# Kernel tuning notes

Measured on AMD Instinct MI355X. Metric: run time of the kernel, lower is better.

The kernel has to match this reference:

```python
import jax, jax.numpy as jnp
import numpy as np

NQ = 12          # qubits per node circuit
DIM = 2 ** NQ    # statevector length 4096


def _apply_1q(state, U, w):
    """Apply 2x2 gate U (shared (2,2) or per-batch (B,2,2)) on wire w. state: (B, 4096)."""
    B = state.shape[0]
    l, r = 2 ** w, 2 ** (NQ - w - 1)
    s = state.reshape(B, l, 2, r)
    if U.ndim == 2:
        s = jnp.einsum('ij,bajc->baic', U, s)
    else:
        s = jnp.einsum('bij,bajc->baic', U, s)
    return s.reshape(B, DIM)


_G = np.zeros((2, 2, 2, 2), np.complex64)  # CNOT tensor: (c_out, t_out, c_in, t_in)
for _c in range(2):
    for _t in range(2):
        _G[_c, _t ^ _c, _c, _t] = 1.0


def _apply_cnot(state, c, t):
    B = state.shape[0]
    lo, hi = min(c, t), max(c, t)
    a, m, r = 2 ** lo, 2 ** (hi - lo - 1), 2 ** (NQ - hi - 1)
    s = state.reshape(B, a, 2, m, 2, r)
    T = _G if c == lo else _G.transpose(1, 0, 3, 2)  # reorder to (lo, hi) axis convention
    s = jnp.einsum('ijkl,bakcld->baicjd', jnp.asarray(T), s)
    return s.reshape(B, DIM)


def _ry_mats(ang):
    """Per-node RY matrices. ang: (B,) -> (B,2,2) complex64."""
    c, s = jnp.cos(ang / 2), jnp.sin(ang / 2)
    U = jnp.stack([jnp.stack([c, -s], -1), jnp.stack([s, c], -1)], -2)
    return U.astype(jnp.complex64)


def _rot_mat(p):
    """PennyLane Rot(phi, theta, omega) = RZ(omega) RY(theta) RZ(phi)."""
    phi, th, om = p[0], p[1], p[2]
    c, s = jnp.cos(th / 2), jnp.sin(th / 2)
    U = jnp.stack([
        jnp.stack([jnp.exp(-0.5j * (phi + om)) * c, -jnp.exp(0.5j * (phi - om)) * s]),
        jnp.stack([jnp.exp(-0.5j * (phi - om)) * s, jnp.exp(0.5j * (phi + om)) * c]),
    ])
    return U.astype(jnp.complex64)


# (rot_wire_a, rot_wire_b, (cnot_control, cnot_target)) blocks of the TTN circuit
_BLOCKS = [(0, 1, (0, 1)), (2, 3, (3, 2)), (4, 5, (4, 5)), (6, 7, (7, 6)),
           (8, 9, (8, 9)), (10, 11, (11, 10)), (1, 2, (1, 2)), (5, 6, (6, 5)),
           (9, 10, (10, 9)), (2, 5, (2, 5)), (5, 9, (5, 9))]


def _ttn_circuit(M, theta):
    """Batched 12-qubit TTN circuit. M: (B,12) angles, theta: (69,). Returns <Z_9>: (B,)."""
    B = M.shape[0]
    state = jnp.zeros((B, DIM), jnp.complex64).at[:, 0].set(1.0)
    for w in range(NQ):
        state = _apply_1q(state, _ry_mats(M[:, w]), w)
    k = 0
    for w1, w2, (c, t) in _BLOCKS:
        state = _apply_1q(state, _rot_mat(theta[3 * k:3 * k + 3]), w1); k += 1
        state = _apply_1q(state, _rot_mat(theta[3 * k:3 * k + 3]), w2); k += 1
        state = _apply_cnot(state, c, t)
    state = _apply_1q(state, _rot_mat(theta[3 * k:3 * k + 3]), 4)  # final Rot, k = 22
    probs = (state.real ** 2 + state.imag ** 2).reshape(B, 2 ** 9, 2, 2 ** 2)
    return probs[:, :, 0].sum((1, 2)) - probs[:, :, 1].sum((1, 2))  # <Z on wire 9>


def setup_inputs() -> dict:
    key = jax.random.key(0)
    kx, ke, ki, ko, kt = jax.random.split(key, 5)
    N, E, D = 1024, 8192, 4
    X = jax.random.normal(kx, (N, D), dtype=jnp.float32)
    e = jax.random.uniform(ke, (E,), dtype=jnp.float32)
    idx_i = jax.random.randint(ki, (E,), 0, N)
    idx_o = jax.random.randint(ko, (E,), 0, N)
    Ri = jnp.zeros((N, E), jnp.float32).at[idx_i, jnp.arange(E)].set(1.0)
    Ro = jnp.zeros((N, E), jnp.float32).at[idx_o, jnp.arange(E)].set(1.0)
    theta = jax.random.uniform(kt, (69,), dtype=jnp.float32, maxval=2 * np.pi)
    return {"X": X, "e": e, "Ri": Ri, "Ro": Ro, "theta": theta}


def reference(X, e, Ri, Ro, theta):
    bo = Ro.T @ X                     # [E, D] features of outgoing nodes
    bi = Ri.T @ X                     # [E, D]
    mi = (Ri * e) @ bo                # [N, D] edge-weighted aggregation
    mo = (Ro * e) @ bi                # [N, D]
    M = jnp.concatenate([mi, mo, X], axis=1)   # [N, 12] -> circuit angles
    z = _ttn_circuit(M, theta)
    return (jnp.pi * (1.0 - z)).astype(jnp.float32)  # 2*pi*(1 - <Z>)/2 per node
```

## Files before the change

### kernel.cpp

```cpp
#include <hip/hip_runtime.h>
#include <math.h>

#define NN 1024
#define NE 8192

struct c32 { float x, y; };
__device__ __forceinline__ c32 cmul(c32 a, c32 b)  { return {a.x*b.x - a.y*b.y, a.x*b.y + a.y*b.x}; }
__device__ __forceinline__ c32 cmulc(c32 a, c32 b) { return {a.x*b.x + a.y*b.y, a.y*b.x - a.x*b.y}; }
__device__ __forceinline__ c32 cadd(c32 a, c32 b)  { return {a.x + b.x, a.y + b.y}; }

__device__ __forceinline__ float sx(float v, int m)  { return __shfl_xor(v, m, 64); }
__device__ __forceinline__ float sidx(float v, int l){ return __shfl(v, l, 64); }

__device__ __forceinline__ void rot2(const float* __restrict__ t3, c32 A[2][2]) {
  float phi = t3[0], th = t3[1], om = t3[2];
  float s, c;   sincosf(0.5f * th, &s, &c);
  float sa, ca; sincosf(0.5f * (phi + om), &sa, &ca);
  float sb, cb; sincosf(0.5f * (phi - om), &sb, &cb);
  A[0][0] = {  ca * c, -sa * c };
  A[0][1] = { -cb * s, -sb * s };
  A[1][0] = {  cb * s, -sb * s };
  A[1][1] = {  ca * c,  sa * c };
}

__global__ void k_extract(const float* __restrict__ Ri, const float* __restrict__ Ro,
                          int* __restrict__ idx_i, int* __restrict__ idx_o,
                          float* __restrict__ mimo) {
  const int per = NN * NE / 4;
  int tid    = blockIdx.x * blockDim.x + threadIdx.x;
  int stride = gridDim.x * blockDim.x;
  if (tid < (2 * NN * 4) / 4) ((float4*)mimo)[tid] = make_float4(0.f, 0.f, 0.f, 0.f);
  for (int t = tid; t < 2 * per; t += stride) {
    bool first = (t < per);
    const float4* src = first ? (const float4*)Ri : (const float4*)Ro;
    int* dst          = first ? idx_i : idx_o;
    int q = first ? t : t - per;
    float4 v = src[q];
    if (v.x != 0.f || v.y != 0.f || v.z != 0.f || v.w != 0.f) {
      int base = q * 4;
      int n = base >> 13;
      int k = base & (NE - 1);
      if (v.x != 0.f) dst[k + 0] = n;
      if (v.y != 0.f) dst[k + 1] = n;
      if (v.z != 0.f) dst[k + 2] = n;
      if (v.w != 0.f) dst[k + 3] = n;
    }
  }
}

__global__ void k_edges(const float* __restrict__ X, const float* __restrict__ e,
                        const int* __restrict__ idx_i, const int* __restrict__ idx_o,
                        float* __restrict__ mi, float* __restrict__ mo) {
  int k = blockIdx.x * blockDim.x + threadIdx.x;
  if (k >= NE) return;
  int ni = idx_i[k], no = idx_o[k];
  float w = e[k];
  float4 xo = ((const float4*)X)[no];
  float4 xi = ((const float4*)X)[ni];
  atomicAdd(&mi[ni * 4 + 0], w * xo.x);
  atomicAdd(&mi[ni * 4 + 1], w * xo.y);
  atomicAdd(&mi[ni * 4 + 2], w * xo.z);
  atomicAdd(&mi[ni * 4 + 3], w * xo.w);
  atomicAdd(&mo[no * 4 + 0], w * xi.x);
  atomicAdd(&mo[no * 4 + 1], w * xi.y);
  atomicAdd(&mo[no * 4 + 2], w * xi.z);
  atomicAdd(&mo[no * 4 + 3], w * xi.w);
}

__device__ __forceinline__ void rot_lane(c32* a, const c32 (*U)[2], int lane, int b) {
  int s = (lane >> b) & 1;
  c32 us = s ? U[1][1] : U[0][0];
  c32 up = s ? U[1][0] : U[0][1];
  #pragma unroll
  for (int r = 0; r < 4; r++) {
    c32 p = { sx(a[r].x, 1 << b), sx(a[r].y, 1 << b) };
    a[r] = cadd(cmul(us, a[r]), cmul(up, p));
  }
}

__device__ __forceinline__ void rot_pair(c32& x0, c32& x1, const c32 (*U)[2]) {
  c32 n0 = cadd(cmul(U[0][0], x0), cmul(U[0][1], x1));
  c32 n1 = cadd(cmul(U[1][0], x0), cmul(U[1][1], x1));
  x0 = n0; x1 = n1;
}

__device__ __forceinline__ void cnot_ll(c32* a, int lane, int c, int t) {
  int idx = lane ^ (((lane >> c) & 1) << t);
  #pragma unroll
  for (int r = 0; r < 4; r++) a[r] = { sidx(a[r].x, idx), sidx(a[r].y, idx) };
}

__device__ __forceinline__ void rotB(c32* bb, const c32 (*U)[2], int k) {
  int mask = (1 << k) - 1;
  #pragma unroll
  for (int t = 0; t < 8; t++) {
    int i0 = ((t & ~mask) << 1) | (t & mask);
    int i1 = i0 | (1 << k);
    c32 b0 = bb[i0], b1 = bb[i1];
    bb[i0] = cadd(cmul(U[0][0], b0), cmul(U[0][1], b1));
    bb[i1] = cadd(cmul(U[1][0], b0), cmul(U[1][1], b1));
  }
}

__device__ __forceinline__ void cnotB(c32* bb, int c, int t) {
  int lo = c < t ? c : t, hi = c < t ? t : c;
  int lm = (1 << lo) - 1, hm = (1 << hi) - 1;
  #pragma unroll
  for (int q = 0; q < 4; q++) {
    int x = ((q & ~lm) << 1) | (q & lm);
    x = ((x & ~hm) << 1) | (x & hm);
    int i0 = x | (1 << c), i1 = i0 | (1 << t);
    c32 tmp = bb[i0]; bb[i0] = bb[i1]; bb[i1] = tmp;
  }
}

__global__ void __launch_bounds__(64) k_sv3(const float* __restrict__ X,
                                            const float* __restrict__ theta,
                                            const float* __restrict__ mi,
                                            const float* __restrict__ mo,
                                            float* __restrict__ out) {
  __shared__ c32 R[23][2][2];
  const int lane = threadIdx.x;
  const int n = blockIdx.x;

  if (lane < 23) {
    c32 A[2][2];
    rot2(theta + 3 * lane, A);
    R[lane][0][0] = A[0][0]; R[lane][0][1] = A[0][1];
    R[lane][1][0] = A[1][0]; R[lane][1][1] = A[1][1];
  }

  float4 miv = ((const float4*)mi)[n];
  float4 mov = ((const float4*)mo)[n];
  float4 xv  = ((const float4*)X)[n];
  float ang[12] = { miv.x, miv.y, miv.z, miv.w, mov.x, mov.y, mov.z, mov.w, xv.x, xv.y, xv.z, xv.w };
  float cw[12], sw[12];
  #pragma unroll
  for (int w = 0; w < 12; w++) __sincosf(0.5f * ang[w], &sw[w], &cw[w]);

  c32 a[4];
  {
    float lfac = 1.f;
    #pragma unroll
    for (int w = 2; w < 8; w++) lfac *= ((lane >> (7 - w)) & 1) ? sw[w] : cw[w];
    a[0] = { cw[0] * cw[1] * lfac, 0.f };
    a[1] = { cw[0] * sw[1] * lfac, 0.f };
    a[2] = { sw[0] * cw[1] * lfac, 0.f };
    a[3] = { sw[0] * sw[1] * lfac, 0.f };
  }
  c32 bb[16];
  #pragma unroll
  for (int i = 0; i < 16; i++) {
    float amp = 1.f;
    #pragma unroll
    for (int w = 8; w < 12; w++) amp *= ((i >> (11 - w)) & 1) ? sw[w] : cw[w];
    bb[i] = { amp, 0.f };
  }
  __syncthreads();

  rot_pair(a[0], a[2], R[0]);  rot_pair(a[1], a[3], R[0]);
  rot_pair(a[0], a[1], R[1]);  rot_pair(a[2], a[3], R[1]);
  { c32 t = a[2]; a[2] = a[3]; a[3] = t; }
  rot_lane(a, R[2], lane, 5);
  rot_lane(a, R[3], lane, 4);
  cnot_ll(a, lane, 4, 5);
  rot_lane(a, R[4], lane, 3);
  rot_lane(a, R[5], lane, 2);
  cnot_ll(a, lane, 3, 2);
  rot_lane(a, R[6], lane, 1);
  rot_lane(a, R[7], lane, 0);
  cnot_ll(a, lane, 0, 1);
  rot_pair(a[0], a[1], R[12]); rot_pair(a[2], a[3], R[12]);
  rot_lane(a, R[13], lane, 5);
  a[1] = { sx(a[1].x, 32), sx(a[1].y, 32) };
  a[3] = { sx(a[3].x, 32), sx(a[3].y, 32) };
  rot_lane(a, R[14], lane, 2);
  rot_lane(a, R[15], lane, 1);
  cnot_ll(a, lane, 1, 2);
  rot_lane(a, R[18], lane, 5);
  rot_lane(a, R[19], lane, 2);
  cnot_ll(a, lane, 5, 2);
  rot_lane(a, R[22], lane, 3);

  rotB(bb, R[8], 3);  rotB(bb, R[9], 2);  cnotB(bb, 3, 2);
  rotB(bb, R[10], 1); rotB(bb, R[11], 0); cnotB(bb, 0, 1);
  rotB(bb, R[16], 2); rotB(bb, R[17], 1); cnotB(bb, 1, 2);

  int s5 = (lane >> 2) & 1;
  float p00 = 0.f, p11 = 0.f; c32 p01 = {0.f, 0.f};
  #pragma unroll
  for (int r = 0; r < 4; r++) {
    c32 pr = { sx(a[r].x, 4), sx(a[r].y, 4) };
    float nn = a[r].x * a[r].x + a[r].y * a[r].y;
    c32 cp = cmulc(a[r], pr);
    p00 += s5 ? 0.f : nn;
    p11 += s5 ? nn : 0.f;
    p01.x += s5 ? 0.f : cp.x;
    p01.y += s5 ? 0.f : cp.y;
  }
  #pragma unroll
  for (int m = 1; m < 64; m <<= 1) {
    p00 += sx(p00, m); p11 += sx(p11, m);
    p01.x += sx(p01.x, m); p01.y += sx(p01.y, m);
  }

  float q00 = 0.f, q11 = 0.f; c32 q01 = {0.f, 0.f};
  #pragma unroll
  for (int ao = 0; ao < 8; ao++) {
    int i0 = ((ao & ~3) << 1) | (ao & 3);
    int i1 = i0 | 4;
    c32 b0 = bb[i0], b1 = bb[i1];
    q00 += b0.x * b0.x + b0.y * b0.y;
    q11 += b1.x * b1.x + b1.y * b1.y;
    q01 = cadd(q01, cmulc(b0, b1));
  }

  c32 U4[4][4];
  #pragma unroll
  for (int i = 0; i < 2; i++)
    #pragma unroll
    for (int p = 0; p < 2; p++)
      #pragma unroll
      for (int j = 0; j < 2; j++)
        #pragma unroll
        for (int q = 0; q < 2; q++)
          U4[2 * i + p][2 * j + q] = cmul(R[20][i][j], R[21][p][q]);
  #pragma unroll
  for (int c = 0; c < 4; c++) { c32 t = U4[2][c]; U4[2][c] = U4[3][c]; U4[3][c] = t; }

  c32 rho5[2][2] = { {{p00, 0.f}, p01}, {{p01.x, -p01.y}, {p11, 0.f}} };
  c32 rho9[2][2] = { {{q00, 0.f}, q01}, {{q01.x, -q01.y}, {q11, 0.f}} };
  float z = 0.f;
  #pragma unroll
  for (int aa = 0; aa < 4; aa++)
    #pragma unroll
    for (int b2 = 0; b2 < 4; b2++) {
      c32 m = {0.f, 0.f};
      #pragma unroll
      for (int i = 0; i < 4; i++) {
        c32 t = cmulc(U4[i][aa], U4[i][b2]);
        if (i & 1) { m.x -= t.x; m.y -= t.y; } else { m = cadd(m, t); }
      }
      c32 rr = cmul(rho5[aa >> 1][b2 >> 1], rho9[aa & 1][b2 & 1]);
      z += m.x * rr.x - m.y * rr.y;
    }

  if (lane == 0) out[n] = 3.14159265358979f * (1.f - z);
}

extern "C" void kernel_launch(void* const* d_in, const int* in_sizes, int n_in,
                              void* d_out, int out_size, void* d_ws, size_t ws_size,
                              hipStream_t stream) {
  (void)in_sizes; (void)n_in; (void)out_size; (void)ws_size;
  const float* X     = (const float*)d_in[0];
  const float* e     = (const float*)d_in[1];
  const float* Ri    = (const float*)d_in[2];
  const float* Ro    = (const float*)d_in[3];
  const float* theta = (const float*)d_in[4];
  float* out = (float*)d_out;

  char* ws = (char*)d_ws;
  int*   idx_i = (int*)(ws);
  int*   idx_o = (int*)(ws + 32768);
  float* mi    = (float*)(ws + 65536);
  float* mo    = (float*)(ws + 65536 + 16384);

  hipLaunchKernelGGL(k_extract, dim3(4096), dim3(256), 0, stream, Ri, Ro, idx_i, idx_o, mi);
  hipLaunchKernelGGL(k_edges,   dim3(NE / 256), dim3(256), 0, stream, X, e, idx_i, idx_o, mi, mo);
  hipLaunchKernelGGL(k_sv3,     dim3(NN), dim3(64), 0, stream, X, theta, mi, mo, out);
}
```

Measured before the change: 40.16 us.

## Fuse extract, edge aggregation and statevector kernels into one cooperative kernel

Replaces the three launches with a single cooperative kernel of 256 blocks that use grid.sync between phases. While scanning Ri and Ro, the kernel pairs each edge's in- and out-node with an atomicExch slot, so the edge aggregation happens inline and the separate index arrays go away. It then runs the circuit with four nodes per 256-thread block. This removes launch gaps and an intermediate pass, but adds grid-wide syncs, atomic exchanges and atomic reads, and uses a smaller grid than before for the dense 64MB scan.

Result: slower. 143.2 us (+256.5%).

```diff
diff --git a/kernel.cpp b/kernel.cpp
--- a/kernel.cpp
+++ b/kernel.cpp
@@ -1,5 +1,8 @@
 #include <hip/hip_runtime.h>
+#include <hip/hip_cooperative_groups.h>
 #include <math.h>
+
+namespace cg = cooperative_groups;
 
 #define NN 1024
 #define NE 8192
@@ -23,50 +26,6 @@
   A[1][1] = {  ca * c,  sa * c };
 }
 
-__global__ void k_extract(const float* __restrict__ Ri, const float* __restrict__ Ro,
-                          int* __restrict__ idx_i, int* __restrict__ idx_o,
-                          float* __restrict__ mimo) {
-  const int per = NN * NE / 4;
-  int tid    = blockIdx.x * blockDim.x + threadIdx.x;
-  int stride = gridDim.x * blockDim.x;
-  if (tid < (2 * NN * 4) / 4) ((float4*)mimo)[tid] = make_float4(0.f, 0.f, 0.f, 0.f);
-  for (int t = tid; t < 2 * per; t += stride) {
-    bool first = (t < per);
-    const float4* src = first ? (const float4*)Ri : (const float4*)Ro;
-    int* dst          = first ? idx_i : idx_o;
-    int q = first ? t : t - per;
-    float4 v = src[q];
-    if (v.x != 0.f || v.y != 0.f || v.z != 0.f || v.w != 0.f) {
-      int base = q * 4;
-      int n = base >> 13;
-      int k = base & (NE - 1);
-      if (v.x != 0.f) dst[k + 0] = n;
-      if (v.y != 0.f) dst[k + 1] = n;
-      if (v.z != 0.f) dst[k + 2] = n;
-      if (v.w != 0.f) dst[k + 3] = n;
-    }
-  }
-}
-
-__global__ void k_edges(const float* __restrict__ X, const float* __restrict__ e,
-                        const int* __restrict__ idx_i, const int* __restrict__ idx_o,
-                        float* __restrict__ mi, float* __restrict__ mo) {
-  int k = blockIdx.x * blockDim.x + threadIdx.x;
-  if (k >= NE) return;
-  int ni = idx_i[k], no = idx_o[k];
-  float w = e[k];
-  float4 xo = ((const float4*)X)[no];
-  float4 xi = ((const float4*)X)[ni];
-  atomicAdd(&mi[ni * 4 + 0], w * xo.x);
-  atomicAdd(&mi[ni * 4 + 1], w * xo.y);
-  atomicAdd(&mi[ni * 4 + 2], w * xo.z);
-  atomicAdd(&mi[ni * 4 + 3], w * xo.w);
-  atomicAdd(&mo[no * 4 + 0], w * xi.x);
-  atomicAdd(&mo[no * 4 + 1], w * xi.y);
-  atomicAdd(&mo[no * 4 + 2], w * xi.z);
-  atomicAdd(&mo[no * 4 + 3], w * xi.w);
-}
-
 __device__ __forceinline__ void rot_lane(c32* a, const c32 (*U)[2], int lane, int b) {
   int s = (lane >> b) & 1;
   c32 us = s ? U[1][1] : U[0][0];
@@ -77,19 +36,16 @@
     a[r] = cadd(cmul(us, a[r]), cmul(up, p));
   }
 }
-
 __device__ __forceinline__ void rot_pair(c32& x0, c32& x1, const c32 (*U)[2]) {
   c32 n0 = cadd(cmul(U[0][0], x0), cmul(U[0][1], x1));
   c32 n1 = cadd(cmul(U[1][0], x0), cmul(U[1][1], x1));
   x0 = n0; x1 = n1;
 }
-
 __device__ __forceinline__ void cnot_ll(c32* a, int lane, int c, int t) {
   int idx = lane ^ (((lane >> c) & 1) << t);
   #pragma unroll
   for (int r = 0; r < 4; r++) a[r] = { sidx(a[r].x, idx), sidx(a[r].y, idx) };
 }
-
 __device__ __forceinline__ void rotB(c32* bb, const c32 (*U)[2], int k) {
   int mask = (1 << k) - 1;
   #pragma unroll
@@ -101,7 +57,6 @@
     bb[i1] = cadd(cmul(U[1][0], b0), cmul(U[1][1], b1));
   }
 }
-
 __device__ __forceinline__ void cnotB(c32* bb, int c, int t) {
   int lo = c < t ? c : t, hi = c < t ? t : c;
   int lm = (1 << lo) - 1, hm = (1 << hi) - 1;
@@ -114,29 +69,124 @@
   }
 }
 
-__global__ void __launch_bounds__(64) k_sv3(const float* __restrict__ X,
-                                            const float* __restrict__ theta,
-                                            const float* __restrict__ mi,
-                                            const float* __restrict__ mo,
-                                            float* __restrict__ out) {
+__device__ __forceinline__ void scanq(float4 v, int q, const float* __restrict__ e,
+                                      const float* __restrict__ X,
+                                      int* __restrict__ slot, float* __restrict__ mimo,
+                                      bool isRo) {
+  if (v.x == 0.f && v.y == 0.f && v.z == 0.f && v.w == 0.f) return;
+  int n = q >> 11;
+  int k = (q << 2) & (NE - 1);
+  float vv[4] = { v.x, v.y, v.z, v.w };
+  #pragma unroll
+  for (int c = 0; c < 4; c++) if (vv[c] != 0.f) {
+    int kk = k + c;
+    int old = atomicExch(&slot[kk], n);
+    if (old >= 0) {
+      float w = e[kk];
+      int ni = isRo ? old : n;
+      int no = isRo ? n : old;
+      float4 xo = ((const float4*)X)[no];
+      float4 xi = ((const float4*)X)[ni];
+      atomicAdd(&mimo[ni * 4 + 0], w * xo.x);
+      atomicAdd(&mimo[ni * 4 + 1], w * xo.y);
+      atomicAdd(&mimo[ni * 4 + 2], w * xo.z);
+      atomicAdd(&mimo[ni * 4 + 3], w * xo.w);
+      atomicAdd(&mimo[4096 + no * 4 + 0], w * xi.x);
+      atomicAdd(&mimo[4096 + no * 4 + 1], w * xi.y);
+      atomicAdd(&mimo[4096 + no * 4 + 2], w * xi.z);
+      atomicAdd(&mimo[4096 + no * 4 + 3], w * xi.w);
+    }
+  }
+}
+
+__global__ void __launch_bounds__(256) k_all(const float* __restrict__ X,
+                                             const float* __restrict__ e,
+                                             const float* __restrict__ Ri,
+                                             const float* __restrict__ Ro,
+                                             const float* __restrict__ theta,
+                                             float* __restrict__ out,
+                                             int* __restrict__ slot,
+                                             float* __restrict__ mimo) {
+  cg::grid_group grid = cg::this_grid();
   __shared__ c32 R[23][2][2];
-  const int lane = threadIdx.x;
-  const int n = blockIdx.x;
-
-  if (lane < 23) {
+  const int tid  = threadIdx.x;
+  const int gtid = blockIdx.x * 256 + tid;
+  const int NT   = 256 * 256;
+
+  if (tid < 23) {
     c32 A[2][2];
-    rot2(theta + 3 * lane, A);
-    R[lane][0][0] = A[0][0]; R[lane][0][1] = A[0][1];
-    R[lane][1][0] = A[1][0]; R[lane][1][1] = A[1][1];
-  }
-
-  float4 miv = ((const float4*)mi)[n];
-  float4 mov = ((const float4*)mo)[n];
-  float4 xv  = ((const float4*)X)[n];
-  float ang[12] = { miv.x, miv.y, miv.z, miv.w, mov.x, mov.y, mov.z, mov.w, xv.x, xv.y, xv.z, xv.w };
+    rot2(theta + 3 * tid, A);
+    R[tid][0][0] = A[0][0]; R[tid][0][1] = A[0][1];
+    R[tid][1][0] = A[1][0]; R[tid][1][1] = A[1][1];
+  }
+  if (gtid < NE) slot[gtid] = -1;
+  if (gtid < 2048) ((float4*)mimo)[gtid] = make_float4(0.f, 0.f, 0.f, 0.f);
+  grid.sync();
+
+  const float4* Ri4 = (const float4*)Ri;
+  const float4* Ro4 = (const float4*)Ro;
+  #pragma unroll 1
+  for (int j = 0; j < 8; j++) {
+    int q0 = gtid + j * 4 * NT;
+    float4 v0 = Ri4[q0], v1 = Ri4[q0 + NT], v2 = Ri4[q0 + 2 * NT], v3 = Ri4[q0 + 3 * NT];
+    scanq(v0, q0, e, X, slot, mimo, false);
+    scanq(v1, q0 + NT, e, X, slot, mimo, false);
+    scanq(v2, q0 + 2 * NT, e, X, slot, mimo, false);
+    scanq(v3, q0 + 3 * NT, e, X, slot, mimo, false);
+  }
+  #pragma unroll 1
+  for (int j = 0; j < 8; j++) {
+    int q0 = gtid + j * 4 * NT;
+    float4 v0 = Ro4[q0], v1 = Ro4[q0 + NT], v2 = Ro4[q0 + 2 * NT], v3 = Ro4[q0 + 3 * NT];
+    scanq(v0, q0, e, X, slot, mimo, true);
+    scanq(v1, q0 + NT, e, X, slot, mimo, true);
+    scanq(v2, q0 + 2 * NT, e, X, slot, mimo, true);
+    scanq(v3, q0 + 3 * NT, e, X, slot, mimo, true);
+  }
+  __threadfence();
+  grid.sync();
+  __threadfence();
+
+  const int lane = tid & 63;
+  const int n = (blockIdx.x << 2) | (tid >> 6);
+
+  float av = 0.f;
+  if (lane < 8) {
+    int off = (lane < 4) ? (n * 4 + lane) : (4096 + n * 4 + (lane - 4));
+    av = atomicAdd(&mimo[off], 0.0f);
+  }
+  float ang[12];
+  #pragma unroll
+  for (int i = 0; i < 8; i++) ang[i] = sidx(av, i);
+  float4 xv = ((const float4*)X)[n];
+  ang[8] = xv.x; ang[9] = xv.y; ang[10] = xv.z; ang[11] = xv.w;
   float cw[12], sw[12];
   #pragma unroll
   for (int w = 0; w < 12; w++) __sincosf(0.5f * ang[w], &sw[w], &cw[w]);
+
+  float q00 = 0.f, q11 = 0.f; c32 q01 = {0.f, 0.f};
+  {
+    c32 bb[16];
+    #pragma unroll
+    for (int i = 0; i < 16; i++) {
+      float amp = 1.f;
+      #pragma unroll
+      for (int w = 8; w < 12; w++) amp *= ((i >> (11 - w)) & 1) ? sw[w] : cw[w];
+      bb[i] = { amp, 0.f };
+    }
+    rotB(bb, R[8], 3);  rotB(bb, R[9], 2);  cnotB(bb, 3, 2);
+    rotB(bb, R[10], 1); rotB(bb, R[11], 0); cnotB(bb, 0, 1);
+    rotB(bb, R[16], 2); rotB(bb, R[17], 1); cnotB(bb, 1, 2);
+    #pragma unroll
+    for (int ao = 0; ao < 8; ao++) {
+      int i0 = ((ao & ~3) << 1) | (ao & 3);
+      int i1 = i0 | 4;
+      c32 b0 = bb[i0], b1 = bb[i1];
+      q00 += b0.x * b0.x + b0.y * b0.y;
+      q11 += b1.x * b1.x + b1.y * b1.y;
+      q01 = cadd(q01, cmulc(b0, b1));
+    }
+  }
 
   c32 a[4];
   {
@@ -148,16 +198,6 @@
     a[2] = { sw[0] * cw[1] * lfac, 0.f };
     a[3] = { sw[0] * sw[1] * lfac, 0.f };
   }
-  c32 bb[16];
-  #pragma unroll
-  for (int i = 0; i < 16; i++) {
-    float amp = 1.f;
-    #pragma unroll
-    for (int w = 8; w < 12; w++) amp *= ((i >> (11 - w)) & 1) ? sw[w] : cw[w];
-    bb[i] = { amp, 0.f };
-  }
-  __syncthreads();
-
   rot_pair(a[0], a[2], R[0]);  rot_pair(a[1], a[3], R[0]);
   rot_pair(a[0], a[1], R[1]);  rot_pair(a[2], a[3], R[1]);
   { c32 t = a[2]; a[2] = a[3]; a[3] = t; }
@@ -182,10 +222,6 @@
   cnot_ll(a, lane, 5, 2);
   rot_lane(a, R[22], lane, 3);
 
-  rotB(bb, R[8], 3);  rotB(bb, R[9], 2);  cnotB(bb, 3, 2);
-  rotB(bb, R[10], 1); rotB(bb, R[11], 0); cnotB(bb, 0, 1);
-  rotB(bb, R[16], 2); rotB(bb, R[17], 1); cnotB(bb, 1, 2);
-
   int s5 = (lane >> 2) & 1;
   float p00 = 0.f, p11 = 0.f; c32 p01 = {0.f, 0.f};
   #pragma unroll
@@ -202,17 +238,6 @@
   for (int m = 1; m < 64; m <<= 1) {
     p00 += sx(p00, m); p11 += sx(p11, m);
     p01.x += sx(p01.x, m); p01.y += sx(p01.y, m);
-  }
-
-  float q00 = 0.f, q11 = 0.f; c32 q01 = {0.f, 0.f};
-  #pragma unroll
-  for (int ao = 0; ao < 8; ao++) {
-    int i0 = ((ao & ~3) << 1) | (ao & 3);
-    int i1 = i0 | 4;
-    c32 b0 = bb[i0], b1 = bb[i1];
-    q00 += b0.x * b0.x + b0.y * b0.y;
-    q11 += b1.x * b1.x + b1.y * b1.y;
-    q01 = cadd(q01, cmulc(b0, b1));
   }
 
   c32 U4[4][4];
@@ -260,12 +285,10 @@
   float* out = (float*)d_out;
 
   char* ws = (char*)d_ws;
-  int*   idx_i = (int*)(ws);
-  int*   idx_o = (int*)(ws + 32768);
-  float* mi    = (float*)(ws + 65536);
-  float* mo    = (float*)(ws + 65536 + 16384);
-
-  hipLaunchKernelGGL(k_extract, dim3(4096), dim3(256), 0, stream, Ri, Ro, idx_i, idx_o, mi);
-  hipLaunchKernelGGL(k_edges,   dim3(NE / 256), dim3(256), 0, stream, X, e, idx_i, idx_o, mi, mo);
-  hipLaunchKernelGGL(k_sv3,     dim3(NN), dim3(64), 0, stream, X, theta, mi, mo, out);
-}
+  int*   slot = (int*)(ws);
+  float* mimo = (float*)(ws + 32768);
+
+  void* args[] = { (void*)&X, (void*)&e, (void*)&Ri, (void*)&Ro, (void*)&theta,
+                   (void*)&out, (void*)&slot, (void*)&mimo };
+  hipLaunchCooperativeKernel((const void*)k_all, dim3(256), dim3(256), args, 0, stream);
+}
```

## Fuse edge aggregation and statevector kernels into one cooperative launch

Applied to the files above, without the earlier changes.

Merges the atomic edge-scatter kernel and the per-node circuit kernel into a single cooperative kernel. A grid-wide sync separates the two phases, and each 256-thread block then handles four nodes, one per wavefront. The aim is to remove one kernel launch and its inter-kernel gap. The cost is a grid sync, atomic-based reads of the aggregated values, and a launch that needs all 256 blocks to be co-resident.

Measured after the change: 103.1 us. +156.7%, slower.

```diff
diff --git a/kernel.cpp b/kernel.cpp
--- a/kernel.cpp
+++ b/kernel.cpp
@@ -1,5 +1,8 @@
 #include <hip/hip_runtime.h>
+#include <hip/hip_cooperative_groups.h>
 #include <math.h>
+
+namespace cg = cooperative_groups;
 
 #define NN 1024
 #define NE 8192
@@ -23,13 +26,56 @@
   A[1][1] = {  ca * c,  sa * c };
 }
 
+__device__ __forceinline__ void rot_lane(c32* a, const c32 (*U)[2], int lane, int b) {
+  int s = (lane >> b) & 1;
+  c32 us = s ? U[1][1] : U[0][0];
+  c32 up = s ? U[1][0] : U[0][1];
+  #pragma unroll
+  for (int r = 0; r < 4; r++) {
+    c32 p = { sx(a[r].x, 1 << b), sx(a[r].y, 1 << b) };
+    a[r] = cadd(cmul(us, a[r]), cmul(up, p));
+  }
+}
+__device__ __forceinline__ void rot_pair(c32& x0, c32& x1, const c32 (*U)[2]) {
+  c32 n0 = cadd(cmul(U[0][0], x0), cmul(U[0][1], x1));
+  c32 n1 = cadd(cmul(U[1][0], x0), cmul(U[1][1], x1));
+  x0 = n0; x1 = n1;
+}
+__device__ __forceinline__ void cnot_ll(c32* a, int lane, int c, int t) {
+  int idx = lane ^ (((lane >> c) & 1) << t);
+  #pragma unroll
+  for (int r = 0; r < 4; r++) a[r] = { sidx(a[r].x, idx), sidx(a[r].y, idx) };
+}
+__device__ __forceinline__ void rotB(c32* bb, const c32 (*U)[2], int k) {
+  int mask = (1 << k) - 1;
+  #pragma unroll
+  for (int t = 0; t < 8; t++) {
+    int i0 = ((t & ~mask) << 1) | (t & mask);
+    int i1 = i0 | (1 << k);
+    c32 b0 = bb[i0], b1 = bb[i1];
+    bb[i0] = cadd(cmul(U[0][0], b0), cmul(U[0][1], b1));
+    bb[i1] = cadd(cmul(U[1][0], b0), cmul(U[1][1], b1));
+  }
+}
+__device__ __forceinline__ void cnotB(c32* bb, int c, int t) {
+  int lo = c < t ? c : t, hi = c < t ? t : c;
+  int lm = (1 << lo) - 1, hm = (1 << hi) - 1;
+  #pragma unroll
+  for (int q = 0; q < 4; q++) {
+    int x = ((q & ~lm) << 1) | (q & lm);
+    x = ((x & ~hm) << 1) | (x & hm);
+    int i0 = x | (1 << c), i1 = i0 | (1 << t);
+    c32 tmp = bb[i0]; bb[i0] = bb[i1]; bb[i1] = tmp;
+  }
+}
+
 __global__ void k_extract(const float* __restrict__ Ri, const float* __restrict__ Ro,
                           int* __restrict__ idx_i, int* __restrict__ idx_o,
                           float* __restrict__ mimo) {
   const int per = NN * NE / 4;
   int tid    = blockIdx.x * blockDim.x + threadIdx.x;
   int stride = gridDim.x * blockDim.x;
-  if (tid < (2 * NN * 4) / 4) ((float4*)mimo)[tid] = make_float4(0.f, 0.f, 0.f, 0.f);
+  if (tid < 2048) ((float4*)mimo)[tid] = make_float4(0.f, 0.f, 0.f, 0.f);
   for (int t = tid; t < 2 * per; t += stride) {
     bool first = (t < per);
     const float4* src = first ? (const float4*)Ri : (const float4*)Ro;
@@ -48,95 +94,83 @@
   }
 }
 
-__global__ void k_edges(const float* __restrict__ X, const float* __restrict__ e,
-                        const int* __restrict__ idx_i, const int* __restrict__ idx_o,
-                        float* __restrict__ mi, float* __restrict__ mo) {
-  int k = blockIdx.x * blockDim.x + threadIdx.x;
-  if (k >= NE) return;
-  int ni = idx_i[k], no = idx_o[k];
-  float w = e[k];
-  float4 xo = ((const float4*)X)[no];
-  float4 xi = ((const float4*)X)[ni];
-  atomicAdd(&mi[ni * 4 + 0], w * xo.x);
-  atomicAdd(&mi[ni * 4 + 1], w * xo.y);
-  atomicAdd(&mi[ni * 4 + 2], w * xo.z);
-  atomicAdd(&mi[ni * 4 + 3], w * xo.w);
-  atomicAdd(&mo[no * 4 + 0], w * xi.x);
-  atomicAdd(&mo[no * 4 + 1], w * xi.y);
-  atomicAdd(&mo[no * 4 + 2], w * xi.z);
-  atomicAdd(&mo[no * 4 + 3], w * xi.w);
-}
-
-__device__ __forceinline__ void rot_lane(c32* a, const c32 (*U)[2], int lane, int b) {
-  int s = (lane >> b) & 1;
-  c32 us = s ? U[1][1] : U[0][0];
-  c32 up = s ? U[1][0] : U[0][1];
-  #pragma unroll
-  for (int r = 0; r < 4; r++) {
-    c32 p = { sx(a[r].x, 1 << b), sx(a[r].y, 1 << b) };
-    a[r] = cadd(cmul(us, a[r]), cmul(up, p));
-  }
-}
-
-__device__ __forceinline__ void rot_pair(c32& x0, c32& x1, const c32 (*U)[2]) {
-  c32 n0 = cadd(cmul(U[0][0], x0), cmul(U[0][1], x1));
-  c32 n1 = cadd(cmul(U[1][0], x0), cmul(U[1][1], x1));
-  x0 = n0; x1 = n1;
-}
-
-__device__ __forceinline__ void cnot_ll(c32* a, int lane, int c, int t) {
-  int idx = lane ^ (((lane >> c) & 1) << t);
-  #pragma unroll
-  for (int r = 0; r < 4; r++) a[r] = { sidx(a[r].x, idx), sidx(a[r].y, idx) };
-}
-
-__device__ __forceinline__ void rotB(c32* bb, const c32 (*U)[2], int k) {
-  int mask = (1 << k) - 1;
-  #pragma unroll
-  for (int t = 0; t < 8; t++) {
-    int i0 = ((t & ~mask) << 1) | (t & mask);
-    int i1 = i0 | (1 << k);
-    c32 b0 = bb[i0], b1 = bb[i1];
-    bb[i0] = cadd(cmul(U[0][0], b0), cmul(U[0][1], b1));
-    bb[i1] = cadd(cmul(U[1][0], b0), cmul(U[1][1], b1));
-  }
-}
-
-__device__ __forceinline__ void cnotB(c32* bb, int c, int t) {
-  int lo = c < t ? c : t, hi = c < t ? t : c;
-  int lm = (1 << lo) - 1, hm = (1 << hi) - 1;
-  #pragma unroll
-  for (int q = 0; q < 4; q++) {
-    int x = ((q & ~lm) << 1) | (q & lm);
-    x = ((x & ~hm) << 1) | (x & hm);
-    int i0 = x | (1 << c), i1 = i0 | (1 << t);
-    c32 tmp = bb[i0]; bb[i0] = bb[i1]; bb[i1] = tmp;
-  }
-}
-
-__global__ void __launch_bounds__(64) k_sv3(const float* __restrict__ X,
+__global__ void __launch_bounds__(256) k_ec(const float* __restrict__ X,
+                                            const float* __restrict__ e,
                                             const float* __restrict__ theta,
-                                            const float* __restrict__ mi,
-                                            const float* __restrict__ mo,
+                                            const int* __restrict__ idx_i,
+                                            const int* __restrict__ idx_o,
+                                            float* __restrict__ mimo,
                                             float* __restrict__ out) {
+  cg::grid_group grid = cg::this_grid();
   __shared__ c32 R[23][2][2];
-  const int lane = threadIdx.x;
-  const int n = blockIdx.x;
-
-  if (lane < 23) {
+  const int tid  = threadIdx.x;
+  const int gtid = blockIdx.x * 256 + tid;
+
+  if (tid < 23) {
     c32 A[2][2];
-    rot2(theta + 3 * lane, A);
-    R[lane][0][0] = A[0][0]; R[lane][0][1] = A[0][1];
-    R[lane][1][0] = A[1][0]; R[lane][1][1] = A[1][1];
-  }
-
-  float4 miv = ((const float4*)mi)[n];
-  float4 mov = ((const float4*)mo)[n];
-  float4 xv  = ((const float4*)X)[n];
-  float ang[12] = { miv.x, miv.y, miv.z, miv.w, mov.x, mov.y, mov.z, mov.w, xv.x, xv.y, xv.z, xv.w };
+    rot2(theta + 3 * tid, A);
+    R[tid][0][0] = A[0][0]; R[tid][0][1] = A[0][1];
+    R[tid][1][0] = A[1][0]; R[tid][1][1] = A[1][1];
+  }
+
+  if (gtid < NE) {
+    int ni = idx_i[gtid], no = idx_o[gtid];
+    float w = e[gtid];
+    float4 xo = ((const float4*)X)[no];
+    float4 xi = ((const float4*)X)[ni];
+    atomicAdd(&mimo[ni * 4 + 0], w * xo.x);
+    atomicAdd(&mimo[ni * 4 + 1], w * xo.y);
+    atomicAdd(&mimo[ni * 4 + 2], w * xo.z);
+    atomicAdd(&mimo[ni * 4 + 3], w * xo.w);
+    atomicAdd(&mimo[4096 + no * 4 + 0], w * xi.x);
+    atomicAdd(&mimo[4096 + no * 4 + 1], w * xi.y);
+    atomicAdd(&mimo[4096 + no * 4 + 2], w * xi.z);
+    atomicAdd(&mimo[4096 + no * 4 + 3], w * xi.w);
+  }
+  __threadfence();
+  grid.sync();
+  __threadfence();
+
+  const int lane = tid & 63;
+  const int n = (blockIdx.x << 2) | (tid >> 6);
+
+  float av = 0.f;
+  if (lane < 8) {
+    int off = (lane < 4) ? (n * 4 + lane) : (4096 + n * 4 + (lane - 4));
+    av = atomicAdd(&mimo[off], 0.0f);
+  }
+  float ang[12];
+  #pragma unroll
+  for (int i = 0; i < 8; i++) ang[i] = sidx(av, i);
+  float4 xv = ((const float4*)X)[n];
+  ang[8] = xv.x; ang[9] = xv.y; ang[10] = xv.z; ang[11] = xv.w;
   float cw[12], sw[12];
   #pragma unroll
   for (int w = 0; w < 12; w++) __sincosf(0.5f * ang[w], &sw[w], &cw[w]);
+
+  float q00 = 0.f, q11 = 0.f; c32 q01 = {0.f, 0.f};
+  {
+    c32 bb[16];
+    #pragma unroll
+    for (int i = 0; i < 16; i++) {
+      float amp = 1.f;
+      #pragma unroll
+      for (int w = 8; w < 12; w++) amp *= ((i >> (11 - w)) & 1) ? sw[w] : cw[w];
+      bb[i] = { amp, 0.f };
+    }
+    rotB(bb, R[8], 3);  rotB(bb, R[9], 2);  cnotB(bb, 3, 2);
+    rotB(bb, R[10], 1); rotB(bb, R[11], 0); cnotB(bb, 0, 1);
+    rotB(bb, R[16], 2); rotB(bb, R[17], 1); cnotB(bb, 1, 2);
+    #pragma unroll
+    for (int ao = 0; ao < 8; ao++) {
+      int i0 = ((ao & ~3) << 1) | (ao & 3);
+      int i1 = i0 | 4;
+      c32 b0 = bb[i0], b1 = bb[i1];
+      q00 += b0.x * b0.x + b0.y * b0.y;
+      q11 += b1.x * b1.x + b1.y * b1.y;
+      q01 = cadd(q01, cmulc(b0, b1));
+    }
+  }
 
   c32 a[4];
   {
@@ -148,16 +182,6 @@
     a[2] = { sw[0] * cw[1] * lfac, 0.f };
     a[3] = { sw[0] * sw[1] * lfac, 0.f };
   }
-  c32 bb[16];
-  #pragma unroll
-  for (int i = 0; i < 16; i++) {
-    float amp = 1.f;
-    #pragma unroll
-    for (int w = 8; w < 12; w++) amp *= ((i >> (11 - w)) & 1) ? sw[w] : cw[w];
-    bb[i] = { amp, 0.f };
-  }
-  __syncthreads();
-
   rot_pair(a[0], a[2], R[0]);  rot_pair(a[1], a[3], R[0]);
   rot_pair(a[0], a[1], R[1]);  rot_pair(a[2], a[3], R[1]);
   { c32 t = a[2]; a[2] = a[3]; a[3] = t; }
@@ -182,10 +206,6 @@
   cnot_ll(a, lane, 5, 2);
   rot_lane(a, R[22], lane, 3);
 
-  rotB(bb, R[8], 3);  rotB(bb, R[9], 2);  cnotB(bb, 3, 2);
-  rotB(bb, R[10], 1); rotB(bb, R[11], 0); cnotB(bb, 0, 1);
-  rotB(bb, R[16], 2); rotB(bb, R[17], 1); cnotB(bb, 1, 2);
-
   int s5 = (lane >> 2) & 1;
   float p00 = 0.f, p11 = 0.f; c32 p01 = {0.f, 0.f};
   #pragma unroll
@@ -202,17 +222,6 @@
   for (int m = 1; m < 64; m <<= 1) {
     p00 += sx(p00, m); p11 += sx(p11, m);
     p01.x += sx(p01.x, m); p01.y += sx(p01.y, m);
-  }
-
-  float q00 = 0.f, q11 = 0.f; c32 q01 = {0.f, 0.f};
-  #pragma unroll
-  for (int ao = 0; ao < 8; ao++) {
-    int i0 = ((ao & ~3) << 1) | (ao & 3);
-    int i1 = i0 | 4;
-    c32 b0 = bb[i0], b1 = bb[i1];
-    q00 += b0.x * b0.x + b0.y * b0.y;
-    q11 += b1.x * b1.x + b1.y * b1.y;
-    q01 = cadd(q01, cmulc(b0, b1));
   }
 
   c32 U4[4][4];
@@ -262,10 +271,11 @@
   char* ws = (char*)d_ws;
   int*   idx_i = (int*)(ws);
   int*   idx_o = (int*)(ws + 32768);
-  float* mi    = (float*)(ws + 65536);
-  float* mo    = (float*)(ws + 65536 + 16384);
-
-  hipLaunchKernelGGL(k_extract, dim3(4096), dim3(256), 0, stream, Ri, Ro, idx_i, idx_o, mi);
-  hipLaunchKernelGGL(k_edges,   dim3(NE / 256), dim3(256), 0, stream, X, e, idx_i, idx_o, mi, mo);
-  hipLaunchKernelGGL(k_sv3,     dim3(NN), dim3(64), 0, stream, X, theta, mi, mo, out);
-}
+  float* mimo  = (float*)(ws + 65536);
+
+  hipLaunchKernelGGL(k_extract, dim3(4096), dim3(256), 0, stream, Ri, Ro, idx_i, idx_o, mimo);
+
+  void* args[] = { (void*)&X, (void*)&e, (void*)&theta, (void*)&idx_i, (void*)&idx_o,
+                   (void*)&mimo, (void*)&out };
+  hipLaunchCooperativeKernel((const void*)k_ec, dim3(256), dim3(256), args, 0, stream);
+}
```
